# Optimization experiments

Hardware: AMD Instinct MI355X
Metric: run time of the kernel (lower is better)

The kernel has to match this reference:

```python
import jax, jax.numpy as jnp
import numpy as np

C = 256      # in_channels
H = 16       # num_heads
K = 7        # tconv kernel size
P1 = 8       # type_1 partition size
P2 = 8       # type_2 partition size
HB = H // 4  # heads per attention branch (= 4)
EPS = 1e-5


def _ln(x, g, b):
    m = x.mean(-1, keepdims=True)
    v = ((x - m) ** 2).mean(-1, keepdims=True)
    return (x - m) / jnp.sqrt(v + EPS) * g + b


def _window_attn(parts, table, heads, P):
    # parts: [B_, P, 3*Cb]; table: [2P-1, heads]
    B_, N, _ = parts.shape
    qkv = parts.reshape(B_, N, 3, heads, -1).transpose(2, 0, 3, 1, 4)  # [3,B_,h,P,d]
    q, k, v = qkv[0], qkv[1], qkv[2]
    scale = heads ** (-0.5)  # NOTE: module scales by num_heads**-0.5 (faithful)
    attn = jnp.einsum('bhnd,bhmd->bhnm', q * scale, k)
    idx = (jnp.arange(P)[:, None] - jnp.arange(P)[None, :]) + P - 1  # [P,P]
    bias = table[idx].transpose(2, 0, 1)  # [h,P,P]
    attn = jax.nn.softmax(attn + bias[None], axis=-1)
    out = jnp.einsum('bhnm,bhmd->bhnd', attn, v)
    return out.transpose(0, 2, 1, 3).reshape(B_, N, -1)


def _type1_part(x, P):  # x: [B,Cc,T] contiguous windows
    B, Cc, T = x.shape
    return x.reshape(B, Cc, T // P, P).transpose(0, 2, 3, 1).reshape(-1, P, Cc)


def _type1_rev(y, B, Cc, T, P):
    return y.reshape(B, T // P, P, Cc).transpose(0, 3, 1, 2).reshape(B, Cc, T)


def _type2_part(x, P):  # strided (dilated) windows
    B, Cc, T = x.shape
    return x.reshape(B, Cc, P, T // P).transpose(0, 3, 2, 1).reshape(-1, P, Cc)


def _type2_rev(y, B, Cc, T, P):
    return y.reshape(B, T // P, P, Cc).transpose(0, 3, 2, 1).reshape(B, Cc, T)


def setup_inputs() -> dict:
    key = jax.random.key(0)
    ks = jax.random.split(key, 16)
    B, T = 16, 8192
    d = {
        'x': jax.random.normal(ks[0], (B, C, T), jnp.float32),
        'g1': jnp.ones((C,), jnp.float32),
        'b1': jnp.zeros((C,), jnp.float32),
        'Wm': jax.random.normal(ks[1], (C, 2 * C), jnp.float32) * 0.02,
        'bm': jnp.zeros((2 * C,), jnp.float32),
        'Wc': jax.random.normal(ks[2], (C // 2, (C // 2) // (H // 2), K), jnp.float32) * 0.05,
        'bc': jnp.zeros((C // 2,), jnp.float32),
        'tab1': jax.random.normal(ks[3], (2 * P1 - 1, HB), jnp.float32) * 0.02,
        'tab2': jax.random.normal(ks[4], (2 * P2 - 1, HB), jnp.float32) * 0.02,
        'Wp': jax.random.normal(ks[5], (C, C), jnp.float32) * 0.02,
        'bp': jnp.zeros((C,), jnp.float32),
        'g2': jnp.ones((C,), jnp.float32),
        'b2': jnp.zeros((C,), jnp.float32),
        'W1': jax.random.normal(ks[6], (C, 4 * C), jnp.float32) * 0.02,
        'bf1': jnp.zeros((4 * C,), jnp.float32),
        'W2': jax.random.normal(ks[7], (4 * C, C), jnp.float32) * 0.02,
        'bf2': jnp.zeros((C,), jnp.float32),
    }
    return d


def _forward(x, g1, b1, Wm, bm, Wc, bc, tab1, tab2, Wp, bp, g2, b2, W1, bf1, W2, bf2):
    B, Cin, T = x.shape
    xt = x.transpose(0, 2, 1)  # [B,T,C]
    skip = xt
    f = (_ln(xt, g1, b1) @ Wm + bm).transpose(0, 2, 1)  # [B,2C,T]
    f_conv, f_attn = f[:, :Cin // 2], f[:, Cin // 2:]
    # grouped temporal conv, padding SAME
    y0 = jax.lax.conv_general_dilated(
        f_conv, Wc, window_strides=(1,), padding=[((K - 1) // 2, (K - 1) // 2)],
        feature_group_count=H // 2, dimension_numbers=('NCH', 'OIH', 'NCH')) + bc[None, :, None]
    Cb3 = 3 * Cin // 4
    fa1, fa2 = f_attn[:, :Cb3], f_attn[:, Cb3:]
    y1 = _type1_rev(_window_attn(_type1_part(fa1, P1), tab1, HB, P1), B, Cin // 4, T, P1)
    y2 = _type2_rev(_window_attn(_type2_part(fa2, P2), tab2, HB, P2), B, Cin // 4, T, P2)
    out = jnp.concatenate([y0, y1, y2], axis=1).transpose(0, 2, 1) @ Wp + bp
    out = skip + out
    h = _ln(out, g2, b2)
    h = jax.nn.gelu(h @ W1 + bf1, approximate=False) @ W2 + bf2
    out = out + h
    return out.transpose(0, 2, 1)  # [B,C,T]


def reference(x, g1, b1, Wm, bm, Wc, bc, tab1, tab2, Wp, bp, g2, b2, W1, bf1, W2, bf2):
    return _forward(x, g1, b1, Wm, bm, Wc, bc, tab1, tab2, Wp, bp, g2, b2, W1, bf1, W2, bf2)
```

## Files before the change

### kernel.cpp

```cpp
#include <hip/hip_runtime.h>
#include <hip/hip_bf16.h>

#define DI __device__ __forceinline__

typedef unsigned short u16;
typedef __attribute__((ext_vector_type(4))) float f32x4;
typedef __attribute__((ext_vector_type(8))) short short8;
typedef __attribute__((ext_vector_type(4))) short short4v;

constexpr int Bb = 16, Tt = 8192;
constexpr int M_TOT = Bb * Tt;

static DI u16 f2bf(float f) {
    union { float f; unsigned u; } v; v.f = f;
    unsigned r = v.u + 0x7fffu + ((v.u >> 16) & 1u);
    return (u16)(r >> 16);
}
static DI float bf2f(u16 u) {
    union { unsigned u; float f; } v; v.u = ((unsigned)u) << 16;
    return v.f;
}
static DI float bf2f_s(short s) { return bf2f((u16)s); }
static DI unsigned pack2bf(float a, float b) {
    return (unsigned)f2bf(a) | ((unsigned)f2bf(b) << 16);
}

static DI void lds_load16(const void* g, void* l) {
    __builtin_amdgcn_global_load_lds(
        (const __attribute__((address_space(1))) void*)g,
        (__attribute__((address_space(3))) void*)l, 16, 0, 0);
}

static DI float gelu_fast(float x) {
    float x2 = x * x;
    float z2 = x * (2.30220723f + 0.10294515f * x2);
    float e;
    asm("v_exp_f32 %0, %1" : "=v"(e) : "v"(z2));
    float r = __builtin_amdgcn_rcpf(1.f + e);
    return x - x * r;
}

__global__ void prep_weights(const float* __restrict__ Wm, const float* __restrict__ Wp,
                             const float* __restrict__ W1, const float* __restrict__ W2,
                             const float* __restrict__ Wc,
                             const float* __restrict__ g1, const float* __restrict__ b1,
                             const float* __restrict__ g2, const float* __restrict__ b2,
                             const float* __restrict__ bm, const float* __restrict__ bf1,
                             u16* __restrict__ WmT, u16* __restrict__ WpT,
                             u16* __restrict__ W1T, u16* __restrict__ W2T,
                             u16* __restrict__ WtC,
                             float* __restrict__ bmF, float* __restrict__ b1F) {
    int i = blockIdx.x * blockDim.x + threadIdx.x;
    int stride = gridDim.x * blockDim.x;
    for (int j = i; j < 512 * 256; j += stride) {
        int n = j >> 8, k = j & 255;
        WmT[j] = f2bf(Wm[k * 512 + n] * g1[k]);
    }
    for (int j = i; j < 256 * 256; j += stride) {
        int n = j >> 8, k = j & 255;
        WpT[j] = f2bf(Wp[k * 256 + n]);
    }
    for (int j = i; j < 1024 * 256; j += stride) {
        int n = j >> 8, k = j & 255;
        W1T[j] = f2bf(W1[k * 1024 + n] * g2[k]);
    }
    for (int j = i; j < 256 * 1024; j += stride) {
        int n = j >> 10, k = j & 1023;
        W2T[j] = f2bf(W2[k * 256 + n]);
    }
    for (int j = i; j < 128 * 128; j += stride) {
        int co = j >> 7, kp = j & 127;
        int tap = kp >> 4, ci = kp & 15;
        float v = (tap < 7) ? Wc[(co * 16 + ci) * 7 + tap] : 0.f;
        WtC[j] = f2bf(v);
    }
    for (int n = i; n < 512; n += stride) {
        float s = bm[n];
        for (int k = 0; k < 256; ++k) s += b1[k] * Wm[k * 512 + n];
        bmF[n] = s;
    }
    for (int n = i; n < 1024; n += stride) {
        float s = bf1[n];
        for (int k = 0; k < 256; ++k) s += b2[k] * W1[k * 1024 + n];
        b1F[n] = s;
    }
}

__global__ __launch_bounds__(256) void ln1_kernel(const float* __restrict__ x,
                                                  u16* __restrict__ xln,
                                                  u16* __restrict__ xt) {
    __shared__ u16 tile[64 * 256];
    __shared__ float ps[64 * 16], pss[64 * 16];
    __shared__ float smean[64], srstd[64];
    int bidx = blockIdx.x;
    int b = bidx >> 7;
    int t0 = (bidx & 127) << 6;
    int tid = threadIdx.x, l = tid & 63, w = tid >> 6;
    int lr = l & 15, lg = l >> 4;
    float s[4] = {}, ss[4] = {};
    #pragma unroll 4
    for (int it = 0; it < 16; ++it) {
        int c = it * 16 + w * 4 + lg;
        f32x4 v = *(const f32x4*)&x[((size_t)b * 256 + c) * 8192 + t0 + lr * 4];
        #pragma unroll
        for (int k = 0; k < 4; ++k) {
            s[k] += v[k]; ss[k] += v[k] * v[k];
            int t = lr * 4 + k;
            int c8 = c >> 3;
            int slot = (c8 & 24) | ((c8 ^ t) & 7);
            tile[t * 256 + slot * 8 + (c & 7)] = f2bf(v[k]);
        }
    }
    #pragma unroll
    for (int k = 0; k < 4; ++k) {
        ps[(lr * 4 + k) * 16 + w * 4 + lg] = s[k];
        pss[(lr * 4 + k) * 16 + w * 4 + lg] = ss[k];
    }
    __syncthreads();
    if (tid < 64) {
        float sum = 0.f, sq = 0.f;
        #pragma unroll
        for (int g = 0; g < 16; ++g) { sum += ps[tid * 16 + g]; sq += pss[tid * 16 + g]; }
        float m = sum * (1.f / 256.f);
        smean[tid] = m;
        srstd[tid] = rsqrtf(sq * (1.f / 256.f) - m * m + 1e-5f);
    }
    __syncthreads();
    int r = tid >> 2, q = tid & 3;
    float m = smean[r], rs = srstd[r];
    size_t rowbase = ((size_t)b * 8192 + t0 + r) * 256;
    #pragma unroll
    for (int u = 0; u < 8; ++u) {
        int c0 = q * 64 + u * 8;
        int c8 = c0 >> 3;
        int slot = (c8 & 24) | ((c8 ^ r) & 7);
        short8 d = *(const short8*)&tile[r * 256 + slot * 8];
        *(short8*)&xt[rowbase + c0] = d;
        short8 o;
        #pragma unroll
        for (int j = 0; j < 8; ++j)
            o[j] = (short)f2bf((bf2f_s(d[j]) - m) * rs);
        *(short8*)&xln[rowbase + c0] = o;
    }
}

template<int EPI, int N, int K>
__global__ __launch_bounds__(256) void gemm_bt2(const u16* __restrict__ A,
                                                const u16* __restrict__ Bt,
                                                const float* __restrict__ bias,
                                                u16* __restrict__ outb,
                                                const u16* __restrict__ skipx) {
    constexpr int NB = N / 128;
    int bid = blockIdx.x;
    int x8 = bid & 7;
    int rest = bid >> 3;
    int ni = rest % NB;
    int mi = (rest / NB) * 8 + x8;
    int m0 = mi * 128, n0 = ni * 128;
    __shared__ u16 As[2][128 * 64];
    __shared__ u16 Bs[2][128 * 64];
    int tid = threadIdx.x, l = tid & 63, w = tid >> 6;
    int mrow = (w >> 1) * 64, ncol = (w & 1) * 64;
    int lr = l & 15, lg = l >> 4;
    f32x4 acc[4][4] = {};
    auto stage = [&](int buf, int k0) {
        #pragma unroll
        for (int p = 0; p < 4; ++p) {
            int cb = p * 256 + w * 64;
            int chunk = cb + l;
            int row = chunk >> 3, k8 = chunk & 7;
            int k8s = k8 ^ (row & 7);
            lds_load16(A  + (size_t)(m0 + row) * K + k0 + k8s * 8, &As[buf][cb * 8]);
            lds_load16(Bt + (size_t)(n0 + row) * K + k0 + k8s * 8, &Bs[buf][cb * 8]);
        }
    };
    stage(0, 0);
    __syncthreads();
    constexpr int NT = K / 64;
    int buf = 0;
    for (int t = 0; t < NT; ++t) {
        if (t + 1 < NT) stage(buf ^ 1, (t + 1) * 64);
        __builtin_amdgcn_s_setprio(1);
        #pragma unroll
        for (int kk = 0; kk < 64; kk += 32) {
            short8 a[4], bfr[4];
            #pragma unroll
            for (int i = 0; i < 4; ++i) {
                int r = mrow + i * 16 + lr;
                a[i] = *(const short8*)&As[buf][r * 64 + ((((kk >> 3) + lg) ^ (r & 7)) << 3)];
            }
            #pragma unroll
            for (int j = 0; j < 4; ++j) {
                int r = ncol + j * 16 + lr;
                bfr[j] = *(const short8*)&Bs[buf][r * 64 + ((((kk >> 3) + lg) ^ (r & 7)) << 3)];
            }
            #pragma unroll
            for (int i = 0; i < 4; ++i)
                #pragma unroll
                for (int j = 0; j < 4; ++j)
                    acc[i][j] = __builtin_amdgcn_mfma_f32_16x16x32_bf16(a[i], bfr[j], acc[i][j], 0, 0, 0);
        }
        __builtin_amdgcn_s_setprio(0);
        __syncthreads();
        buf ^= 1;
    }
    #pragma unroll
    for (int i = 0; i < 4; ++i) {
        int row0 = m0 + mrow + i * 16 + lg * 4;
        #pragma unroll
        for (int j = 0; j < 4; ++j) {
            int col = n0 + ncol + j * 16 + lr;
            float bv = bias[col];
            f32x4 v = acc[i][j];
            if constexpr (EPI == 0) {
                #pragma unroll
                for (int r = 0; r < 4; ++r)
                    outb[(size_t)(row0 + r) * N + col] = f2bf(v[r] + bv);
            } else {
                #pragma unroll
                for (int r = 0; r < 4; ++r)
                    outb[(size_t)(row0 + r) * N + col] =
                        f2bf(v[r] + bv + bf2f(skipx[(size_t)(row0 + r) * 256 + col]));
            }
        }
    }
}

__global__ __launch_bounds__(512) void ffn_fused2(const u16* __restrict__ outb,
                                                  const u16* __restrict__ W1g,
                                                  const float* __restrict__ b1F,
                                                  const u16* __restrict__ W2T,
                                                  const float* __restrict__ bf2v,
                                                  float* __restrict__ out) {
    __shared__ u16 W1c[2][64 * 256];
    __shared__ u16 W2c[2][256 * 64];
    __shared__ u16 hbuf[128 * 64];
    int bid = blockIdx.x;
    int m0 = bid * 128;
    int tid = threadIdx.x, l = tid & 63, w = tid >> 6;
    int lr = l & 15, lg = l >> 4;
    int wm = w >> 1, wn = w & 1;

    short8 a_reg[2][8];
    float mean[2], rstd[2];
    #pragma unroll
    for (int mt = 0; mt < 2; ++mt) {
        size_t base = (size_t)(m0 + wm * 32 + mt * 16 + lr) * 256 + lg * 8;
        float s = 0.f, ss = 0.f;
        #pragma unroll
        for (int ks = 0; ks < 8; ++ks) {
            short8 rv = *(const short8*)&outb[base + ks * 32];
            a_reg[mt][ks] = rv;
            #pragma unroll
            for (int e = 0; e < 8; ++e) { float v = bf2f_s(rv[e]); s += v; ss += v * v; }
        }
        s += __shfl_xor(s, 16); ss += __shfl_xor(ss, 16);
        s += __shfl_xor(s, 32); ss += __shfl_xor(ss, 32);
        float m = s * (1.f / 256.f);
        mean[mt] = m;
        rstd[mt] = rsqrtf(ss * (1.f / 256.f) - m * m + 1e-5f);
    }
    #pragma unroll
    for (int mt = 0; mt < 2; ++mt) {
        float m = mean[mt], rs = rstd[mt];
        #pragma unroll
        for (int ks = 0; ks < 8; ++ks) {
            short8 rv = a_reg[mt][ks], ov;
            #pragma unroll
            for (int e = 0; e < 8; ++e) ov[e] = (short)f2bf((bf2f_s(rv[e]) - m) * rs);
            a_reg[mt][ks] = ov;
        }
    }

    auto stageW1 = [&](int buf, int c) {
        #pragma unroll
        for (int p = 0; p < 4; ++p) {
            int cb = p * 512 + w * 64;
            int chunk = cb + l;
            int row = chunk >> 5, sl = chunk & 31;
            int sl2 = (sl & 24) | ((sl ^ row) & 7);
            lds_load16(W1g + (size_t)(c * 64 + row) * 256 + sl2 * 8, &W1c[buf][cb * 8]);
        }
    };
    auto stageW2 = [&](int buf, int c) {
        #pragma unroll
        for (int p = 0; p < 4; ++p) {
            int cb = p * 512 + w * 64;
            int chunk = cb + l;
            int row = chunk >> 3, sl = chunk & 7;
            int sl2 = sl ^ (row & 7);
            lds_load16(W2T + (size_t)row * 1024 + c * 64 + sl2 * 8, &W2c[buf][cb * 8]);
        }
    };
    stageW1(0, 0); stageW2(0, 0);
    f32x4 acc2[2][8] = {};
    __syncthreads();

    for (int c = 0; c < 16; ++c) {
        int buf = c & 1;
        if (c < 15) { stageW1(buf ^ 1, c + 1); stageW2(buf ^ 1, c + 1); }
        f32x4 acc1[2][2] = {};
        __builtin_amdgcn_s_setprio(1);
        #pragma unroll
        for (int ks = 0; ks < 8; ++ks) {
            short8 wf[2];
            #pragma unroll
            for (int nt = 0; nt < 2; ++nt) {
                int n = wn * 32 + nt * 16 + lr;
                int sl = ks * 4 + lg;
                int sl2 = (sl & 24) | ((sl ^ n) & 7);
                wf[nt] = *(const short8*)&W1c[buf][n * 256 + sl2 * 8];
            }
            #pragma unroll
            for (int nt = 0; nt < 2; ++nt)
                #pragma unroll
                for (int mt = 0; mt < 2; ++mt)
                    acc1[nt][mt] = __builtin_amdgcn_mfma_f32_16x16x32_bf16(
                        wf[nt], a_reg[mt][ks], acc1[nt][mt], 0, 0, 0);
        }
        __builtin_amdgcn_s_setprio(0);
        #pragma unroll
        for (int nt = 0; nt < 2; ++nt) {
            int colb = wn * 32 + nt * 16 + lg * 4;
            f32x4 bv4 = *(const f32x4*)&b1F[c * 64 + colb];
            #pragma unroll
            for (int mt = 0; mt < 2; ++mt) {
                int row = wm * 32 + mt * 16 + lr;
                unsigned d0 = pack2bf(gelu_fast(acc1[nt][mt][0] + bv4[0]),
                                      gelu_fast(acc1[nt][mt][1] + bv4[1]));
                unsigned d1 = pack2bf(gelu_fast(acc1[nt][mt][2] + bv4[2]),
                                      gelu_fast(acc1[nt][mt][3] + bv4[3]));
                int s0 = colb >> 3;
                int sl2 = s0 ^ (row & 7);
                *(unsigned*)&hbuf[row * 64 + sl2 * 8 + (colb & 7)] = d0;
                *(unsigned*)&hbuf[row * 64 + sl2 * 8 + (colb & 7) + 2] = d1;
            }
        }
        __syncthreads();
        __builtin_amdgcn_s_setprio(1);
        #pragma unroll
        for (int ks = 0; ks < 2; ++ks) {
            short8 hf[2], w2f[8];
            #pragma unroll
            for (int mt = 0; mt < 2; ++mt) {
                int row = wm * 32 + mt * 16 + lr;
                int sl2 = (ks * 4 + lg) ^ (row & 7);
                hf[mt] = *(const short8*)&hbuf[row * 64 + sl2 * 8];
            }
            #pragma unroll
            for (int nt = 0; nt < 8; ++nt) {
                int n = wn * 128 + nt * 16 + lr;
                int sl2 = (ks * 4 + lg) ^ (n & 7);
                w2f[nt] = *(const short8*)&W2c[buf][n * 64 + sl2 * 8];
            }
            #pragma unroll
            for (int mt = 0; mt < 2; ++mt)
                #pragma unroll
                for (int nt = 0; nt < 8; ++nt)
                    acc2[mt][nt] = __builtin_amdgcn_mfma_f32_16x16x32_bf16(
                        hf[mt], w2f[nt], acc2[mt][nt], 0, 0, 0);
        }
        __builtin_amdgcn_s_setprio(0);
        __syncthreads();
    }
    int bb_ = m0 >> 13;
    int tb = m0 & 8191;
    #pragma unroll
    for (int mt = 0; mt < 2; ++mt) {
        int row0 = wm * 32 + mt * 16 + lg * 4;
        #pragma unroll
        for (int nt = 0; nt < 8; ++nt) {
            int col = wn * 128 + nt * 16 + lr;
            float bv = bf2v[col];
            f32x4 o;
            #pragma unroll
            for (int r = 0; r < 4; ++r)
                o[r] = acc2[mt][nt][r] + bv + bf2f(outb[(size_t)(m0 + row0 + r) * 256 + col]);
            *(f32x4*)&out[((size_t)bb_ * 256 + col) * 8192 + tb + row0] = o;
        }
    }
}

__global__ __launch_bounds__(256) void conv_kernel(const u16* __restrict__ f,
                                                   const u16* __restrict__ WtC,
                                                   const float* __restrict__ bc,
                                                   u16* __restrict__ att) {
    __shared__ u16 fs[72 * 128];
    __shared__ u16 wt[128 * 128];
    int bid = blockIdx.x;
    int b = bid >> 7;
    int t0 = (bid & 127) << 6;
    int tid = threadIdx.x, l = tid & 63, w = tid >> 6;
    for (int c = tid; c < 2048; c += 256) {
        int row = c >> 4, c8 = c & 15;
        int slot = (c8 & 8) | ((c8 ^ row) & 7);
        *(uint4*)&wt[row * 128 + slot * 8] = *(const uint4*)&WtC[c * 8];
    }
    for (int c = tid; c < 72 * 16; c += 256) {
        int rrow = c >> 4, c8 = c & 15;
        int t = t0 - 3 + rrow;
        uint4 v = {0u, 0u, 0u, 0u};
        if (t >= 0 && t < 8192)
            v = *(const uint4*)&f[((size_t)b * 8192 + t) * 512 + c8 * 8];
        int slot = (c8 & 8) | ((c8 ^ rrow) & 7);
        *(uint4*)&fs[rrow * 128 + slot * 8] = v;
    }
    __syncthreads();
    int wr = w >> 1, wc = w & 1;
    int lr = l & 15, lg = l >> 4;
    f32x4 acc[2][4] = {};
    #pragma unroll
    for (int kk = 0; kk < 4; ++kk) {
        int kp = kk * 32 + lg * 8;
        int tap = kp >> 4, ci = kp & 15;
        #pragma unroll
        for (int i = 0; i < 2; ++i) {
            int trow = wr * 32 + i * 16 + lr;
            #pragma unroll
            for (int g = 0; g < 4; ++g) {
                int ra = trow + tap;
                int ea = (wc * 4 + g) * 2 + (ci >> 3);
                short8 a = *(const short8*)&fs[ra * 128 + (((ea & 8) | ((ea ^ ra) & 7)) << 3)];
                int nb = (wc * 4 + g) * 16 + lr;
                int eb = kp >> 3;
                short8 bfr = *(const short8*)&wt[nb * 128 + (((eb & 8) | ((eb ^ nb) & 7)) << 3)];
                acc[i][g] = __builtin_amdgcn_mfma_f32_16x16x32_bf16(a, bfr, acc[i][g], 0, 0, 0);
            }
        }
    }
    #pragma unroll
    for (int i = 0; i < 2; ++i) {
        int trow = wr * 32 + i * 16 + lg * 4;
        #pragma unroll
        for (int g = 0; g < 4; ++g) {
            int co = (wc * 4 + g) * 16 + lr;
            float bv = bc[co];
            #pragma unroll
            for (int r = 0; r < 4; ++r) {
                int t = t0 + trow + r;
                att[((size_t)b * 8192 + t) * 256 + co] = f2bf(acc[i][g][r] + bv);
            }
        }
    }
}

template<int TYPE>
__global__ __launch_bounds__(256) void attn_kernel(const u16* __restrict__ f,
                                                   const float* __restrict__ tab,
                                                   u16* __restrict__ att) {
    __shared__ u16 qkv[64 * 200];
    __shared__ float stab[60];
    constexpr int QBASE = (TYPE == 1) ? 128 : 320;
    constexpr int OBASE = (TYPE == 1) ? 128 : 192;
    int bid = blockIdx.x;
    int b = bid >> 7;
    int j0 = (bid & 127) << 3;
    int tid = threadIdx.x;
    if (tid < 60) stab[tid] = tab[tid];
    for (int c = tid; c < 64 * 24; c += 256) {
        int ridx = c / 24, off = (c % 24) << 3;
        int wl = ridx >> 3, n = ridx & 7;
        int t = (TYPE == 1) ? ((j0 + wl) * 8 + n) : (n * 1024 + j0 + wl);
        *(uint4*)&qkv[ridx * 200 + off] = *(const uint4*)&f[((size_t)b * 8192 + t) * 512 + QBASE + off];
    }
    __syncthreads();
    int wl = tid >> 5, h = (tid >> 3) & 3, n = tid & 7;
    const u16* qr = &qkv[(wl * 8 + n) * 200 + h * 16];
    float q[16];
    {
        short8 q0 = *(const short8*)qr, q1 = *(const short8*)(qr + 8);
        #pragma unroll
        for (int d = 0; d < 8; ++d) { q[d] = bf2f_s(q0[d]); q[d + 8] = bf2f_s(q1[d]); }
    }
    float s[8];
    #pragma unroll
    for (int m = 0; m < 8; ++m) {
        const u16* kr = &qkv[(wl * 8 + m) * 200 + 64 + h * 16];
        short8 k0 = *(const short8*)kr, k1 = *(const short8*)(kr + 8);
        float a = 0.f;
        #pragma unroll
        for (int d = 0; d < 8; ++d) a += q[d] * bf2f_s(k0[d]) + q[d + 8] * bf2f_s(k1[d]);
        s[m] = 0.5f * a + stab[(n - m + 7) * 4 + h];
    }
    float mx = s[0];
    #pragma unroll
    for (int m = 1; m < 8; ++m) mx = fmaxf(mx, s[m]);
    float sum = 0.f;
    #pragma unroll
    for (int m = 0; m < 8; ++m) { s[m] = __expf(s[m] - mx); sum += s[m]; }
    float rinv = 1.f / sum;
    float o[16] = {};
    #pragma unroll
    for (int m = 0; m < 8; ++m) {
        float p = s[m] * rinv;
        const u16* vr = &qkv[(wl * 8 + m) * 200 + 128 + h * 16];
        short8 v0 = *(const short8*)vr, v1 = *(const short8*)(vr + 8);
        #pragma unroll
        for (int d = 0; d < 8; ++d) { o[d] += p * bf2f_s(v0[d]); o[d + 8] += p * bf2f_s(v1[d]); }
    }
    int t = (TYPE == 1) ? ((j0 + wl) * 8 + n) : (n * 1024 + j0 + wl);
    short8 o0, o1;
    #pragma unroll
    for (int d = 0; d < 8; ++d) { o0[d] = (short)f2bf(o[d]); o1[d] = (short)f2bf(o[d + 8]); }
    u16* op = &att[((size_t)b * 8192 + t) * 256 + OBASE + h * 16];
    *(short8*)op = o0; *(short8*)(op + 8) = o1;
}

extern "C" void kernel_launch(void* const* d_in, const int* in_sizes, int n_in,
                              void* d_out, int out_size, void* d_ws, size_t ws_size,
                              hipStream_t stream) {
    const float* x    = (const float*)d_in[0];
    const float* g1   = (const float*)d_in[1];
    const float* b1   = (const float*)d_in[2];
    const float* Wm   = (const float*)d_in[3];
    const float* bm   = (const float*)d_in[4];
    const float* Wc   = (const float*)d_in[5];
    const float* bc   = (const float*)d_in[6];
    const float* tab1 = (const float*)d_in[7];
    const float* tab2 = (const float*)d_in[8];
    const float* Wp   = (const float*)d_in[9];
    const float* bp   = (const float*)d_in[10];
    const float* g2   = (const float*)d_in[11];
    const float* b2   = (const float*)d_in[12];
    const float* W1   = (const float*)d_in[13];
    const float* bf1  = (const float*)d_in[14];
    const float* W2   = (const float*)d_in[15];
    const float* bf2  = (const float*)d_in[16];
    float* out = (float*)d_out;

    char* ws = (char*)d_ws;
    u16* f    = (u16*)(ws);
    u16* att  = (u16*)(ws + 134217728);
    u16* outb = (u16*)(ws + 201326592);
    u16* xlnb = (u16*)(ws + 268435456);
    u16* xt   = (u16*)(ws + 335544320);
    char* wb = ws + 402653184;
    u16* WmT   = (u16*)wb;
    u16* WpT   = (u16*)(wb + 262144);
    u16* W1T   = (u16*)(wb + 393216);
    u16* W2T   = (u16*)(wb + 917504);
    u16* WtC   = (u16*)(wb + 1441792);
    float* bmF = (float*)(wb + 1474560);
    float* b1F = (float*)(wb + 1476608);

    prep_weights<<<512, 256, 0, stream>>>(Wm, Wp, W1, W2, Wc, g1, b1, g2, b2, bm, bf1,
                                          WmT, WpT, W1T, W2T, WtC, bmF, b1F);
    ln1_kernel<<<Bb * (Tt / 64), 256, 0, stream>>>(x, xlnb, xt);
    gemm_bt2<0, 512, 256><<<(M_TOT / 128) * 4, 256, 0, stream>>>(xlnb, WmT, bmF, f, nullptr);
    conv_kernel<<<Bb * (Tt / 64), 256, 0, stream>>>(f, WtC, bc, att);
    attn_kernel<1><<<Bb * 128, 256, 0, stream>>>(f, tab1, att);
    attn_kernel<2><<<Bb * 128, 256, 0, stream>>>(f, tab2, att);
    gemm_bt2<1, 256, 256><<<(M_TOT / 128) * 2, 256, 0, stream>>>(att, WpT, bp, outb, xt);
    ffn_fused2<<<M_TOT / 128, 512, 0, stream>>>(outb, W1T, b1F, W2T, bf2, out);
}
```

Before: 524.5 us.

## Single-buffer FFN weight tiles in LDS and stage between GEMM phases

```diff
diff --git a/kernel.cpp b/kernel.cpp
--- a/kernel.cpp
+++ b/kernel.cpp
@@ -226,14 +226,14 @@
     }
 }
 
-__global__ __launch_bounds__(512) void ffn_fused2(const u16* __restrict__ outb,
+__global__ __launch_bounds__(512) void ffn_fused3(const u16* __restrict__ outb,
                                                   const u16* __restrict__ W1g,
                                                   const float* __restrict__ b1F,
                                                   const u16* __restrict__ W2T,
                                                   const float* __restrict__ bf2v,
                                                   float* __restrict__ out) {
-    __shared__ u16 W1c[2][64 * 256];
-    __shared__ u16 W2c[2][256 * 64];
+    __shared__ u16 W1c[64 * 256];
+    __shared__ u16 W2c[256 * 64];
     __shared__ u16 hbuf[128 * 64];
     int bid = blockIdx.x;
     int m0 = bid * 128;
@@ -272,33 +272,31 @@
         }
     }
 
-    auto stageW1 = [&](int buf, int c) {
+    auto stageW1 = [&](int c) {
         #pragma unroll
         for (int p = 0; p < 4; ++p) {
             int cb = p * 512 + w * 64;
             int chunk = cb + l;
             int row = chunk >> 5, sl = chunk & 31;
             int sl2 = (sl & 24) | ((sl ^ row) & 7);
-            lds_load16(W1g + (size_t)(c * 64 + row) * 256 + sl2 * 8, &W1c[buf][cb * 8]);
+            lds_load16(W1g + (size_t)(c * 64 + row) * 256 + sl2 * 8, &W1c[cb * 8]);
         }
     };
-    auto stageW2 = [&](int buf, int c) {
+    auto stageW2 = [&](int c) {
         #pragma unroll
         for (int p = 0; p < 4; ++p) {
             int cb = p * 512 + w * 64;
             int chunk = cb + l;
             int row = chunk >> 3, sl = chunk & 7;
             int sl2 = sl ^ (row & 7);
-            lds_load16(W2T + (size_t)row * 1024 + c * 64 + sl2 * 8, &W2c[buf][cb * 8]);
+            lds_load16(W2T + (size_t)row * 1024 + c * 64 + sl2 * 8, &W2c[cb * 8]);
         }
     };
-    stageW1(0, 0); stageW2(0, 0);
+    stageW1(0); stageW2(0);
     f32x4 acc2[2][8] = {};
     __syncthreads();
 
     for (int c = 0; c < 16; ++c) {
-        int buf = c & 1;
-        if (c < 15) { stageW1(buf ^ 1, c + 1); stageW2(buf ^ 1, c + 1); }
         f32x4 acc1[2][2] = {};
         __builtin_amdgcn_s_setprio(1);
         #pragma unroll
@@ -309,7 +307,7 @@
                 int n = wn * 32 + nt * 16 + lr;
                 int sl = ks * 4 + lg;
                 int sl2 = (sl & 24) | ((sl ^ n) & 7);
-                wf[nt] = *(const short8*)&W1c[buf][n * 256 + sl2 * 8];
+                wf[nt] = *(const short8*)&W1c[n * 256 + sl2 * 8];
             }
             #pragma unroll
             for (int nt = 0; nt < 2; ++nt)
@@ -326,17 +324,19 @@
             #pragma unroll
             for (int mt = 0; mt < 2; ++mt) {
                 int row = wm * 32 + mt * 16 + lr;
-                unsigned d0 = pack2bf(gelu_fast(acc1[nt][mt][0] + bv4[0]),
-                                      gelu_fast(acc1[nt][mt][1] + bv4[1]));
-                unsigned d1 = pack2bf(gelu_fast(acc1[nt][mt][2] + bv4[2]),
-                                      gelu_fast(acc1[nt][mt][3] + bv4[3]));
-                int s0 = colb >> 3;
-                int sl2 = s0 ^ (row & 7);
-                *(unsigned*)&hbuf[row * 64 + sl2 * 8 + (colb & 7)] = d0;
-                *(unsigned*)&hbuf[row * 64 + sl2 * 8 + (colb & 7) + 2] = d1;
-            }
-        }
-        __syncthreads();
+                uint2 dd;
+                dd.x = pack2bf(gelu_fast(acc1[nt][mt][0] + bv4[0]),
+                               gelu_fast(acc1[nt][mt][1] + bv4[1]));
+                dd.y = pack2bf(gelu_fast(acc1[nt][mt][2] + bv4[2]),
+                               gelu_fast(acc1[nt][mt][3] + bv4[3]));
+                int sl2 = (colb >> 3) ^ (row & 7);
+                *(uint2*)&hbuf[row * 64 + sl2 * 8 + (colb & 7)] = dd;
+            }
+        }
+        asm volatile("s_waitcnt lgkmcnt(0)" ::: "memory");
+        __builtin_amdgcn_s_barrier();
+        __builtin_amdgcn_sched_barrier(0);
+        if (c < 15) stageW1(c + 1);
         __builtin_amdgcn_s_setprio(1);
         #pragma unroll
         for (int ks = 0; ks < 2; ++ks) {
@@ -351,7 +351,7 @@
             for (int nt = 0; nt < 8; ++nt) {
                 int n = wn * 128 + nt * 16 + lr;
                 int sl2 = (ks * 4 + lg) ^ (n & 7);
-                w2f[nt] = *(const short8*)&W2c[buf][n * 64 + sl2 * 8];
+                w2f[nt] = *(const short8*)&W2c[n * 64 + sl2 * 8];
             }
             #pragma unroll
             for (int mt = 0; mt < 2; ++mt)
@@ -361,6 +361,10 @@
                         hf[mt], w2f[nt], acc2[mt][nt], 0, 0, 0);
         }
         __builtin_amdgcn_s_setprio(0);
+        asm volatile("s_waitcnt lgkmcnt(0)" ::: "memory");
+        __builtin_amdgcn_s_barrier();
+        __builtin_amdgcn_sched_barrier(0);
+        if (c < 15) stageW2(c + 1);
         __syncthreads();
     }
     int bb_ = m0 >> 13;
@@ -551,5 +555,5 @@
     attn_kernel<1><<<Bb * 128, 256, 0, stream>>>(f, tab1, att);
     attn_kernel<2><<<Bb * 128, 256, 0, stream>>>(f, tab2, att);
     gemm_bt2<1, 256, 256><<<(M_TOT / 128) * 2, 256, 0, stream>>>(att, WpT, bp, outb, xt);
-    ffn_fused2<<<M_TOT / 128, 512, 0, stream>>>(outb, W1T, b1F, W2T, bf2, out);
-}
+    ffn_fused3<<<M_TOT / 128, 512, 0, stream>>>(outb, W1T, b1F, W2T, bf2, out);
+}
```

After: 529.8 us. Within noise of the previous version (+1.0%).
